# Kernel tuning notes

Measured on AMD Instinct MI355X. Metric: run time of the kernel, lower is better.

The kernel has to match this reference:

```python
import jax, jax.numpy as jnp
import numpy as np

IN_F, HID, OUT_F, NVIRT = 256, 64, 128, 1
H1, H2 = 2, 1  # heads per GAT layer


def gat_conv(x, src, dst, W, a_src, a_dst, b, n_seg, concat):
    """PyG-style GATConv: per-edge attention, segment-softmax over dst, scatter-add."""
    H, C = a_src.shape
    h = (x @ W).reshape(-1, H, C)                      # (N, H, C)
    es = jnp.einsum('nhc,hc->nh', h, a_src)            # (N, H)
    ed = jnp.einsum('nhc,hc->nh', h, a_dst)
    e = jax.nn.leaky_relu(es[src] + ed[dst], 0.2)      # (E, H)
    emax = jax.ops.segment_max(e, dst, num_segments=n_seg)
    ee = jnp.exp(e - emax[dst])
    den = jax.ops.segment_sum(ee, dst, num_segments=n_seg)
    alpha = ee / den[dst]                              # (E, H)
    out = jax.ops.segment_sum(h[src] * alpha[:, :, None], dst, num_segments=n_seg)
    out = out.reshape(n_seg, H * C) if concat else out.mean(axis=1)
    return out + b


def setup_inputs() -> dict:
    key = jax.random.key(0)
    ks = jax.random.split(key, 16)
    N, E = 50000, 800000
    node_features = jax.random.normal(ks[0], (N, IN_F), dtype=jnp.float32)
    edge_index = jax.random.randint(ks[1], (2, E), 0, N, dtype=jnp.int32)
    s1 = 1.0 / np.sqrt(IN_F)
    s2 = 1.0 / np.sqrt(H1 * HID)
    sj = 1.0 / np.sqrt(IN_F + H1 * HID + OUT_F)
    return {
        'node_features': node_features,
        'edge_index': edge_index,
        'num_nodes': N,
        'virtual_emb': jax.random.normal(ks[2], (NVIRT, IN_F), dtype=jnp.float32),
        'W1': jax.random.normal(ks[3], (IN_F, H1 * HID), dtype=jnp.float32) * s1,
        'a1_src': jax.random.normal(ks[4], (H1, HID), dtype=jnp.float32) * s1,
        'a1_dst': jax.random.normal(ks[5], (H1, HID), dtype=jnp.float32) * s1,
        'b1': jnp.zeros((H1 * HID,), dtype=jnp.float32),
        'W2': jax.random.normal(ks[6], (H1 * HID, H2 * OUT_F), dtype=jnp.float32) * s2,
        'a2_src': jax.random.normal(ks[7], (H2, OUT_F), dtype=jnp.float32) * s2,
        'a2_dst': jax.random.normal(ks[8], (H2, OUT_F), dtype=jnp.float32) * s2,
        'b2': jnp.zeros((OUT_F,), dtype=jnp.float32),
        'Wj': jax.random.normal(ks[9], (IN_F + H1 * HID + OUT_F, OUT_F), dtype=jnp.float32) * sj,
        'bj': jnp.zeros((OUT_F,), dtype=jnp.float32),
    }


def reference(node_features, edge_index, num_nodes, virtual_emb, W1, a1_src,
              a1_dst, b1, W2, a2_src, a2_dst, b2, Wj, bj):
    N = num_nodes
    V = virtual_emb.shape[0]
    aug_x = jnp.concatenate([node_features, virtual_emb], axis=0)   # (N+V, in)
    # virtual edges: every real node -> each virtual node
    vsrc = jnp.tile(jnp.arange(N, dtype=edge_index.dtype), V)
    vdst = N + jnp.repeat(jnp.arange(V, dtype=edge_index.dtype), N)
    src = jnp.concatenate([edge_index[0], vsrc])
    dst = jnp.concatenate([edge_index[1], vdst])
    h1 = jax.nn.elu(gat_conv(aug_x, src, dst, W1, a1_src, a1_dst, b1, N + V, True))
    h2 = gat_conv(h1, src, dst, W2, a2_src, a2_dst, b2, N + V, False)
    comb = jnp.concatenate([node_features, h1[:N], h2[:N]], axis=1)
    return comb @ Wj + bj
```

## Files before the change

kernel.cpp:

```cpp
#include <hip/hip_runtime.h>
#include <hip/hip_bf16.h>
#include <math.h>


#define NF_IN 256

__global__ __launch_bounds__(256) void hist_kernel(
    const int* __restrict__ dst, int* __restrict__ deg, int E)
{
    int e = blockIdx.x * 256 + threadIdx.x;
    if (e < E) atomicAdd(&deg[dst[e]], 1);
}

__global__ __launch_bounds__(256) void scan_partial(
    const int* __restrict__ deg, int* __restrict__ bsum, int N)
{
    __shared__ int sm[256];
    int i = blockIdx.x * 256 + threadIdx.x;
    int v = (i < N) ? deg[i] : 0;
    sm[threadIdx.x] = v;
    __syncthreads();
    for (int off = 128; off > 0; off >>= 1) {
        if (threadIdx.x < off) sm[threadIdx.x] += sm[threadIdx.x + off];
        __syncthreads();
    }
    if (threadIdx.x == 0) bsum[blockIdx.x] = sm[0];
}

__global__ __launch_bounds__(1024) void scan_bsum(
    int* __restrict__ bsum, int nb, int* __restrict__ rowptr, int N, int E)
{
    __shared__ int sm[1024];
    int t = threadIdx.x;
    int v = (t < nb) ? bsum[t] : 0;
    sm[t] = v;
    __syncthreads();
    for (int off = 1; off < 1024; off <<= 1) {
        int x = (t >= off) ? sm[t - off] : 0;
        __syncthreads();
        sm[t] += x;
        __syncthreads();
    }
    if (t < nb) bsum[t] = sm[t] - v;
    if (t == 0) rowptr[N] = E;
}

__global__ __launch_bounds__(256) void scan_final(
    const int* __restrict__ deg, const int* __restrict__ bsum,
    int* __restrict__ rowptr, int N)
{
    __shared__ int sm[256];
    int t = threadIdx.x;
    int i = blockIdx.x * 256 + t;
    int v = (i < N) ? deg[i] : 0;
    sm[t] = v;
    __syncthreads();
    for (int off = 1; off < 256; off <<= 1) {
        int x = (t >= off) ? sm[t - off] : 0;
        __syncthreads();
        sm[t] += x;
        __syncthreads();
    }
    if (i < N) rowptr[i] = sm[t] - v + bsum[blockIdx.x];
}

__global__ __launch_bounds__(256) void fill_kernel(
    const int* __restrict__ src, const int* __restrict__ dst,
    const int* __restrict__ rowptr, int* __restrict__ cur,
    int* __restrict__ csr_src, int E)
{
    int e = blockIdx.x * 256 + threadIdx.x;
    if (e >= E) return;
    int d = dst[e];
    int pos = rowptr[d] + atomicAdd(&cur[d], 1);
    csr_src[pos] = src[e];
}

__global__ __launch_bounds__(128) void gemm1_kernel(
    const float* __restrict__ x, const float* __restrict__ W1,
    const float* __restrict__ a1s, const float* __restrict__ a1d,
    float* __restrict__ h_a, float* __restrict__ es1, float* __restrict__ ed1,
    int N)
{
    __shared__ float4 xs[8][64];
    const int t = threadIdx.x;
    const int base = blockIdx.x * 8;
    const float4* x4 = (const float4*)x;
    for (int idx = t; idx < 8 * 64; idx += 128) {
        int r = idx >> 6, kk = idx & 63;
        int row = base + r;
        xs[r][kk] = (row < N) ? x4[(size_t)row * 64 + kk] : make_float4(0.f, 0.f, 0.f, 0.f);
    }
    __syncthreads();

    float acc[8] = {0.f, 0.f, 0.f, 0.f, 0.f, 0.f, 0.f, 0.f};
    const int j = t;
    for (int k4 = 0; k4 < 64; ++k4) {
        const int k = k4 * 4;
        float w0 = W1[(k + 0) * 128 + j];
        float w1 = W1[(k + 1) * 128 + j];
        float w2 = W1[(k + 2) * 128 + j];
        float w3 = W1[(k + 3) * 128 + j];
#pragma unroll
        for (int r = 0; r < 8; ++r) {
            float4 xv = xs[r][k4];
            acc[r] = fmaf(xv.x, w0, acc[r]);
            acc[r] = fmaf(xv.y, w1, acc[r]);
            acc[r] = fmaf(xv.z, w2, acc[r]);
            acc[r] = fmaf(xv.w, w3, acc[r]);
        }
    }

    const float as = a1s[j];
    const float ad = a1d[j];
    const int head = j >> 6;
    const int lane = j & 63;
#pragma unroll
    for (int r = 0; r < 8; ++r) {
        int row = base + r;
        if (row < N) h_a[(size_t)row * 128 + j] = acc[r];
        float es = acc[r] * as;
        float ed = acc[r] * ad;
#pragma unroll
        for (int off = 32; off > 0; off >>= 1) {
            es += __shfl_xor(es, off, 64);
            ed += __shfl_xor(ed, off, 64);
        }
        if (row < N && lane == 0) {
            es1[row * 2 + head] = es;
            ed1[row * 2 + head] = ed;
        }
    }
}

__global__ __launch_bounds__(256) void gather1_kernel(
    const int* __restrict__ rowptr, const int* __restrict__ csr_src,
    const float* __restrict__ es1, const float* __restrict__ ed1,
    const float* __restrict__ h_a, const float* __restrict__ b1,
    float* __restrict__ h1, int N)
{
    int node = blockIdx.x * 4 + (threadIdx.x >> 6);
    if (node >= N) return;
    int lane = threadIdx.x & 63;
    int head = lane >> 5;
    float edh = ed1[node * 2 + head];
    int b = rowptr[node], e = rowptr[node + 1];
    float acc0 = 0.f, acc1 = 0.f, den = 0.f;
    int s = (b < e) ? csr_src[b] : 0;
    for (int i = b; i < e; ++i) {
        int snext = (i + 1 < e) ? csr_src[i + 1] : 0;
        float ev = es1[s * 2 + head] + edh;
        ev = ev > 0.f ? ev : 0.2f * ev;
        float w = expf(ev);
        float2 hv = *(const float2*)&h_a[(size_t)s * 128 + lane * 2];
        acc0 = fmaf(w, hv.x, acc0);
        acc1 = fmaf(w, hv.y, acc1);
        den += w;
        s = snext;
    }
    float inv = den > 0.f ? 1.f / den : 0.f;
    float2 bb = *(const float2*)&b1[lane * 2];
    float v0 = acc0 * inv + bb.x;
    float v1 = acc1 * inv + bb.y;
    v0 = v0 > 0.f ? v0 : expm1f(v0);
    v1 = v1 > 0.f ? v1 : expm1f(v1);
    *(float2*)&h1[(size_t)node * 128 + lane * 2] = make_float2(v0, v1);
}

__global__ __launch_bounds__(128) void gemm2_kernel(
    const float* __restrict__ h1, const float* __restrict__ W2,
    const float* __restrict__ a2s, const float* __restrict__ a2d,
    float* __restrict__ h_b, float* __restrict__ es2, float* __restrict__ ed2,
    int N)
{
    __shared__ float4 xs[8][32];
    __shared__ float red[2][8][2];
    const int t = threadIdx.x;
    const int base = blockIdx.x * 8;
    const float4* x4 = (const float4*)h1;
    for (int idx = t; idx < 8 * 32; idx += 128) {
        int r = idx >> 5, kk = idx & 31;
        int row = base + r;
        xs[r][kk] = (row < N) ? x4[(size_t)row * 32 + kk] : make_float4(0.f, 0.f, 0.f, 0.f);
    }
    __syncthreads();

    float acc[8] = {0.f, 0.f, 0.f, 0.f, 0.f, 0.f, 0.f, 0.f};
    const int j = t;
    for (int k4 = 0; k4 < 32; ++k4) {
        const int k = k4 * 4;
        float w0 = W2[(k + 0) * 128 + j];
        float w1 = W2[(k + 1) * 128 + j];
        float w2 = W2[(k + 2) * 128 + j];
        float w3 = W2[(k + 3) * 128 + j];
#pragma unroll
        for (int r = 0; r < 8; ++r) {
            float4 xv = xs[r][k4];
            acc[r] = fmaf(xv.x, w0, acc[r]);
            acc[r] = fmaf(xv.y, w1, acc[r]);
            acc[r] = fmaf(xv.z, w2, acc[r]);
            acc[r] = fmaf(xv.w, w3, acc[r]);
        }
    }

    const float as = a2s[j];
    const float ad = a2d[j];
    const int wave = j >> 6;
    const int lane = j & 63;
#pragma unroll
    for (int r = 0; r < 8; ++r) {
        int row = base + r;
        if (row < N) h_b[(size_t)row * 128 + j] = acc[r];
        float es = acc[r] * as;
        float ed = acc[r] * ad;
#pragma unroll
        for (int off = 32; off > 0; off >>= 1) {
            es += __shfl_xor(es, off, 64);
            ed += __shfl_xor(ed, off, 64);
        }
        if (lane == 0) {
            red[wave][r][0] = es;
            red[wave][r][1] = ed;
        }
    }
    __syncthreads();
    if (t < 16) {
        int r = t >> 1, which = t & 1;
        int row = base + r;
        if (row < N) {
            float v = red[0][r][which] + red[1][r][which];
            if (which == 0) es2[row] = v; else ed2[row] = v;
        }
    }
}

__global__ __launch_bounds__(256) void gather2_kernel(
    const int* __restrict__ rowptr, const int* __restrict__ csr_src,
    const float* __restrict__ es2, const float* __restrict__ ed2,
    const float* __restrict__ h_b, const float* __restrict__ b2,
    float* __restrict__ h2n, int N)
{
    int node = blockIdx.x * 4 + (threadIdx.x >> 6);
    if (node >= N) return;
    int lane = threadIdx.x & 63;
    float edh = ed2[node];
    int b = rowptr[node], e = rowptr[node + 1];
    float acc0 = 0.f, acc1 = 0.f, den = 0.f;
    int s = (b < e) ? csr_src[b] : 0;
    for (int i = b; i < e; ++i) {
        int snext = (i + 1 < e) ? csr_src[i + 1] : 0;
        float ev = es2[s] + edh;
        ev = ev > 0.f ? ev : 0.2f * ev;
        float w = expf(ev);
        float2 hv = *(const float2*)&h_b[(size_t)s * 128 + lane * 2];
        acc0 = fmaf(w, hv.x, acc0);
        acc1 = fmaf(w, hv.y, acc1);
        den += w;
        s = snext;
    }
    float inv = den > 0.f ? 1.f / den : 0.f;
    float2 bb = *(const float2*)&b2[lane * 2];
    *(float2*)&h2n[(size_t)node * 128 + lane * 2] =
        make_float2(acc0 * inv + bb.x, acc1 * inv + bb.y);
}

__global__ __launch_bounds__(128) void final_kernel(
    const float* __restrict__ x, const float* __restrict__ h1,
    const float* __restrict__ h2n, const float* __restrict__ Wj,
    const float* __restrict__ bj, float* __restrict__ out, int N)
{
    __shared__ float xs[8][512];
    const int t = threadIdx.x;
    const int base = blockIdx.x * 8;
#pragma unroll
    for (int r = 0; r < 8; ++r) {
        int row = base + r;
        bool v = row < N;
        xs[r][t]       = v ? x[(size_t)row * 256 + t] : 0.f;
        xs[r][128 + t] = v ? x[(size_t)row * 256 + 128 + t] : 0.f;
        xs[r][256 + t] = v ? h1[(size_t)row * 128 + t] : 0.f;
        xs[r][384 + t] = v ? h2n[(size_t)row * 128 + t] : 0.f;
    }
    __syncthreads();

    float acc[8] = {0.f, 0.f, 0.f, 0.f, 0.f, 0.f, 0.f, 0.f};
    for (int k4 = 0; k4 < 128; ++k4) {
        const int k = k4 * 4;
        float w0 = Wj[(k + 0) * 128 + t];
        float w1 = Wj[(k + 1) * 128 + t];
        float w2 = Wj[(k + 2) * 128 + t];
        float w3 = Wj[(k + 3) * 128 + t];
#pragma unroll
        for (int r = 0; r < 8; ++r) {
            float4 xv = *(const float4*)&xs[r][k];
            acc[r] = fmaf(xv.x, w0, acc[r]);
            acc[r] = fmaf(xv.y, w1, acc[r]);
            acc[r] = fmaf(xv.z, w2, acc[r]);
            acc[r] = fmaf(xv.w, w3, acc[r]);
        }
    }
    float bb = bj[t];
#pragma unroll
    for (int r = 0; r < 8; ++r) {
        int row = base + r;
        if (row < N) out[(size_t)row * 128 + t] = acc[r] + bb;
    }
}

extern "C" void kernel_launch(void* const* d_in, const int* in_sizes, int n_in,
                              void* d_out, int out_size, void* d_ws, size_t ws_size,
                              hipStream_t stream)
{
    const float* x   = (const float*)d_in[0];
    const int*   ei  = (const int*)d_in[1];
    const float* W1  = (const float*)d_in[4];
    const float* a1s = (const float*)d_in[5];
    const float* a1d = (const float*)d_in[6];
    const float* b1  = (const float*)d_in[7];
    const float* W2  = (const float*)d_in[8];
    const float* a2s = (const float*)d_in[9];
    const float* a2d = (const float*)d_in[10];
    const float* b2  = (const float*)d_in[11];
    const float* Wj  = (const float*)d_in[12];
    const float* bj  = (const float*)d_in[13];
    float* out = (float*)d_out;

    const int N = in_sizes[0] / NF_IN;
    const int E = in_sizes[1] / 2;
    const int* src = ei;
    const int* dst = ei + E;

    char* wp = (char*)d_ws;
    size_t nb = (size_t)N * 128;
    float* h_a  = (float*)wp; wp += nb * sizeof(float);
    float* h1   = (float*)wp; wp += nb * sizeof(float);
    float* h2n  = (float*)wp; wp += nb * sizeof(float);
    float* es1  = (float*)wp; wp += 2 * (size_t)N * sizeof(float);
    float* ed1  = (float*)wp; wp += 2 * (size_t)N * sizeof(float);
    float* es2  = (float*)wp; wp += (size_t)N * sizeof(float);
    float* ed2  = (float*)wp; wp += (size_t)N * sizeof(float);
    int* deg    = (int*)wp;   wp += (size_t)N * sizeof(int);
    int* cur    = (int*)wp;   wp += (size_t)N * sizeof(int);
    int* rowptr = (int*)wp;   wp += ((size_t)N + 1) * sizeof(int);
    int* bsum   = (int*)wp;   wp += 1024 * sizeof(int);
    int* csr_src= (int*)wp;   wp += (size_t)E * sizeof(int);

    const int NB = (N + 255) / 256;
    const int edgeBlocks = (E + 255) / 256;
    const int rowBlocks = (N + 7) / 8;
    const int nodeBlocks = (N + 3) / 4;

    hipMemsetAsync(deg, 0, 2 * (size_t)N * sizeof(int), stream);
    hist_kernel<<<edgeBlocks, 256, 0, stream>>>(dst, deg, E);
    scan_partial<<<NB, 256, 0, stream>>>(deg, bsum, N);
    scan_bsum<<<1, 1024, 0, stream>>>(bsum, NB, rowptr, N, E);
    scan_final<<<NB, 256, 0, stream>>>(deg, bsum, rowptr, N);
    fill_kernel<<<edgeBlocks, 256, 0, stream>>>(src, dst, rowptr, cur, csr_src, E);

    gemm1_kernel<<<rowBlocks, 128, 0, stream>>>(x, W1, a1s, a1d, h_a, es1, ed1, N);
    gather1_kernel<<<nodeBlocks, 256, 0, stream>>>(rowptr, csr_src, es1, ed1, h_a, b1, h1, N);
    gemm2_kernel<<<rowBlocks, 128, 0, stream>>>(h1, W2, a2s, a2d, h_a, es2, ed2, N);
    gather2_kernel<<<nodeBlocks, 256, 0, stream>>>(rowptr, csr_src, es2, ed2, h_a, b2, h2n, N);
    final_kernel<<<rowBlocks, 128, 0, stream>>>(x, h1, h2n, Wj, bj, out, N);
}
```

Before: 646.6 us.

## Tile final projection GEMM with shared-memory A/B tiles and 8x4 register blocking

Rewrites the final concat-and-project kernel as a classic tiled SGEMM: 64 rows per block, K tiles of 64 staged in shared memory (A transposed, Wj slab), and each thread computes an 8x4 output micro-tile. The old kernel reloaded Wj from global memory for every 8-row block, with one output per thread per row. The new one cuts Wj traffic and raises FMA-per-load intensity. In exchange it uses more shared memory and registers, and the transposed A stores may bank-conflict.

```diff
diff --git a/kernel.cpp b/kernel.cpp
--- a/kernel.cpp
+++ b/kernel.cpp
@@ -264,46 +264,76 @@
         make_float2(acc0 * inv + bb.x, acc1 * inv + bb.y);
 }
 
-__global__ __launch_bounds__(128) void final_kernel(
+__global__ __launch_bounds__(256) void final_kernel(
     const float* __restrict__ x, const float* __restrict__ h1,
     const float* __restrict__ h2n, const float* __restrict__ Wj,
     const float* __restrict__ bj, float* __restrict__ out, int N)
 {
-    __shared__ float xs[8][512];
-    const int t = threadIdx.x;
-    const int base = blockIdx.x * 8;
+    __shared__ float At[64][64];
+    __shared__ float Bs[64][128];
+
+    const int t  = threadIdx.x;
+    const int tx = t & 31;
+    const int ty = t >> 5;
+    const int rowbase = blockIdx.x * 64;
+
+    float acc[8][4] = {};
+
+    for (int k0 = 0; k0 < 512; k0 += 64) {
+        const float* sp; int width;
+        if (k0 < 256)      { sp = x   + k0;         width = 256; }
+        else if (k0 < 384) { sp = h1  + (k0 - 256); width = 128; }
+        else               { sp = h2n + (k0 - 384); width = 128; }
+
+        {
+            int r  = t >> 2;
+            int kq = (t & 3) * 16;
+            int row = rowbase + r;
+#pragma unroll
+            for (int i = 0; i < 4; ++i) {
+                int kl = kq + i * 4;
+                float4 v = (row < N)
+                    ? *(const float4*)&sp[(size_t)row * width + kl]
+                    : make_float4(0.f, 0.f, 0.f, 0.f);
+                At[kl + 0][r] = v.x;
+                At[kl + 1][r] = v.y;
+                At[kl + 2][r] = v.z;
+                At[kl + 3][r] = v.w;
+            }
+        }
+#pragma unroll
+        for (int j = 0; j < 8; ++j) {
+            int idx = t + j * 256;
+            int kk = idx >> 5, c4 = idx & 31;
+            *(float4*)&Bs[kk][c4 * 4] =
+                *(const float4*)&Wj[(size_t)(k0 + kk) * 128 + c4 * 4];
+        }
+        __syncthreads();
+
+        for (int kk = 0; kk < 64; ++kk) {
+            float4 b4 = *(const float4*)&Bs[kk][tx * 4];
+            float4 a0 = *(const float4*)&At[kk][ty * 8];
+            float4 a1 = *(const float4*)&At[kk][ty * 8 + 4];
+            float a[8] = {a0.x, a0.y, a0.z, a0.w, a1.x, a1.y, a1.z, a1.w};
+            float b[4] = {b4.x, b4.y, b4.z, b4.w};
+#pragma unroll
+            for (int r = 0; r < 8; ++r)
+#pragma unroll
+                for (int c = 0; c < 4; ++c)
+                    acc[r][c] = fmaf(a[r], b[c], acc[r][c]);
+        }
+        __syncthreads();
+    }
+
+    float4 bb = *(const float4*)&bj[tx * 4];
 #pragma unroll
     for (int r = 0; r < 8; ++r) {
-        int row = base + r;
-        bool v = row < N;
-        xs[r][t]       = v ? x[(size_t)row * 256 + t] : 0.f;
-        xs[r][128 + t] = v ? x[(size_t)row * 256 + 128 + t] : 0.f;
-        xs[r][256 + t] = v ? h1[(size_t)row * 128 + t] : 0.f;
-        xs[r][384 + t] = v ? h2n[(size_t)row * 128 + t] : 0.f;
-    }
-    __syncthreads();
-
-    float acc[8] = {0.f, 0.f, 0.f, 0.f, 0.f, 0.f, 0.f, 0.f};
-    for (int k4 = 0; k4 < 128; ++k4) {
-        const int k = k4 * 4;
-        float w0 = Wj[(k + 0) * 128 + t];
-        float w1 = Wj[(k + 1) * 128 + t];
-        float w2 = Wj[(k + 2) * 128 + t];
-        float w3 = Wj[(k + 3) * 128 + t];
-#pragma unroll
-        for (int r = 0; r < 8; ++r) {
-            float4 xv = *(const float4*)&xs[r][k];
-            acc[r] = fmaf(xv.x, w0, acc[r]);
-            acc[r] = fmaf(xv.y, w1, acc[r]);
-            acc[r] = fmaf(xv.z, w2, acc[r]);
-            acc[r] = fmaf(xv.w, w3, acc[r]);
-        }
-    }
-    float bb = bj[t];
-#pragma unroll
-    for (int r = 0; r < 8; ++r) {
-        int row = base + r;
-        if (row < N) out[(size_t)row * 128 + t] = acc[r] + bb;
+        int row = rowbase + ty * 8 + r;
+        if (row < N) {
+            float4 o = make_float4(acc[r][0] + bb.x, acc[r][1] + bb.y,
+                                   acc[r][2] + bb.z, acc[r][3] + bb.w);
+            *(float4*)&out[(size_t)row * 128 + tx * 4] = o;
+        }
     }
 }
 
@@ -349,6 +379,7 @@
     const int edgeBlocks = (E + 255) / 256;
     const int rowBlocks = (N + 7) / 8;
     const int nodeBlocks = (N + 3) / 4;
+    const int finalBlocks = (N + 63) / 64;
 
     hipMemsetAsync(deg, 0, 2 * (size_t)N * sizeof(int), stream);
     hist_kernel<<<edgeBlocks, 256, 0, stream>>>(dst, deg, E);
@@ -361,5 +392,5 @@
     gather1_kernel<<<nodeBlocks, 256, 0, stream>>>(rowptr, csr_src, es1, ed1, h_a, b1, h1, N);
     gemm2_kernel<<<rowBlocks, 128, 0, stream>>>(h1, W2, a2s, a2d, h_a, es2, ed2, N);
     gather2_kernel<<<nodeBlocks, 256, 0, stream>>>(rowptr, csr_src, es2, ed2, h_a, b2, h2n, N);
-    final_kernel<<<rowBlocks, 128, 0, stream>>>(x, h1, h2n, Wj, bj, out, N);
-}
+    final_kernel<<<finalBlocks, 256, 0, stream>>>(x, h1, h2n, Wj, bj, out, N);
+}
```

New measurement: 604.2 us. -6.6%, faster.
